# Performance work log

Measured on AMD Instinct MI355X. Metric: run time of the kernel, lower is better.

## Reference

```python
import jax, jax.numpy as jnp
import numpy as np

N, E, IN_DIM, OUT_DIM = 12288, 6144, 256, 256


def setup_inputs() -> dict:
    key = jax.random.key(0)
    k1, k2, k3, k4, k5 = jax.random.split(key, 5)
    x = jax.random.normal(k1, (N, IN_DIM), dtype=jnp.float32)
    # incidence-like matrix (dense, values in [0,1))
    H = jax.random.uniform(k2, (N, E), dtype=jnp.float32)
    # degree-normalizer diagonals: positive entries on the diagonal
    dv = jax.random.uniform(k3, (N,), dtype=jnp.float32, minval=0.1, maxval=1.0)
    de = jax.random.uniform(k4, (E,), dtype=jnp.float32, minval=0.1, maxval=1.0)
    D_v_neg_sqrt = jnp.diag(dv)
    D_e_neg = jnp.diag(de)
    # Linear params (xavier-like weight, zero bias)
    W = jax.random.normal(k5, (IN_DIM, OUT_DIM), dtype=jnp.float32) * (1.0 / np.sqrt(IN_DIM))
    b = jnp.zeros((OUT_DIM,), dtype=jnp.float32)
    return {"x": x, "H": H, "D_v_neg_sqrt": D_v_neg_sqrt, "D_e_neg": D_e_neg, "W": W, "b": b}


def reference(x, H, D_v_neg_sqrt, D_e_neg, W, b):
    # x_transformed = Linear(x)
    x_t = x @ W + b                      # [N, out]
    x_norm = D_v_neg_sqrt @ x_t          # [N, out]
    x_he = H.T @ x_norm                  # [E, out]
    x_he_norm = D_e_neg @ x_he           # [E, out]
    x_node = H @ x_he_norm               # [N, out]
    out = D_v_neg_sqrt @ x_node          # [N, out]
    # dropout is identity in eval mode
    return out
```

## Files before the change

kernel.cpp:

```cpp
#include <hip/hip_runtime.h>

#define NN 12288
#define NE 6144
#define ND 256

typedef __attribute__((ext_vector_type(8))) short short8;
typedef __attribute__((ext_vector_type(4))) float f32x4;
typedef unsigned short u16;
typedef unsigned int u32;

__device__ inline u16 f2bf(float f) {
  union { float f; u32 u; } v; v.f = f;
  u32 r = v.u + 0x7fffu + ((v.u >> 16) & 1u);
  return (u16)(r >> 16);
}

__device__ inline void gll16(const void* g, void* l) {
  __builtin_amdgcn_global_load_lds(
      (const __attribute__((address_space(1))) u32*)g,
      (__attribute__((address_space(3))) u32*)l, 16, 0, 0);
}

__device__ inline void stage_B(const u16* __restrict__ Bg, int ldb, int k0,
                               u16* __restrict__ Blds) {
  const int w = threadIdx.x >> 6;
  const int lane = threadIdx.x & 63;
  const int dd = lane >> 2, p = lane & 3;
#pragma unroll
  for (int s = 0; s < 4; ++s) {
    const int dbase = (w * 4 + s) * 16;
    const int n = dbase + dd;
    const int c = (p - (n >> 1)) & 3;
    gll16(Bg + (size_t)n * ldb + k0 + c * 8, Blds + dbase * 32);
  }
}

__device__ inline short8 load_B(const u16* __restrict__ Blds, int n, int quad) {
  const int p = (quad + (n >> 1)) & 3;
  return *(const short8*)(Blds + n * 32 + p * 8);
}

__device__ inline void compute_tile(const u16* __restrict__ Al,
                                    const u16* __restrict__ Bl, int w, int ln,
                                    int quad, f32x4 (&acc)[4][4]) {
  short8 af[4];
#pragma unroll
  for (int mt = 0; mt < 4; ++mt)
    af[mt] = *(const short8*)(Al + (mt * 16 + ln) * 40 + quad * 8);
#pragma unroll
  for (int nt = 0; nt < 4; ++nt) {
    short8 bf = load_B(Bl, w * 64 + nt * 16 + ln, quad);
#pragma unroll
    for (int mt = 0; mt < 4; ++mt)
      acc[nt][mt] = __builtin_amdgcn_mfma_f32_16x16x32_bf16(af[mt], bf, acc[nt][mt], 0, 0, 0);
  }
}

__device__ inline short8 pack8(float4 f0, float4 f1) {
  short8 av;
  av[0] = (short)f2bf(f0.x); av[1] = (short)f2bf(f0.y);
  av[2] = (short)f2bf(f0.z); av[3] = (short)f2bf(f0.w);
  av[4] = (short)f2bf(f1.x); av[5] = (short)f2bf(f1.y);
  av[6] = (short)f2bf(f1.z); av[7] = (short)f2bf(f1.w);
  return av;
}

__global__ __launch_bounds__(256) void k_xform(
    const float* __restrict__ x, const u16* __restrict__ Wt,
    const float* __restrict__ b, const float* __restrict__ dv,
    u16* __restrict__ xnt) {
  __shared__ u16 Alds[64 * 40];
  __shared__ u16 Blds[256 * 32];
  const int tid = threadIdx.x;
  const int w = tid >> 6, lane = tid & 63, ln = lane & 15, quad = lane >> 4;
  const int m0 = blockIdx.x * 64;
  const int am = tid >> 2, ac = (tid & 3) * 8;
  f32x4 acc[4][4] = {};
  for (int kt = 0; kt < ND / 32; ++kt) {
    const int k0 = kt * 32;
    __syncthreads();
    stage_B(Wt, ND, k0, Blds);
    const float4* pa = (const float4*)(x + (size_t)(m0 + am) * ND + k0 + ac);
    *(short8*)(Alds + am * 40 + ac) = pack8(pa[0], pa[1]);
    __syncthreads();
    compute_tile(Alds, Blds, w, ln, quad, acc);
  }
#pragma unroll
  for (int nt = 0; nt < 4; ++nt) {
    const int d = w * 64 + nt * 16 + ln;
    const float bb = b[d];
#pragma unroll
    for (int mt = 0; mt < 4; ++mt) {
      const int vb = m0 + mt * 16 + quad * 4;
      f32x4 a = acc[nt][mt];
      union { u16 h[4]; uint2 u; } pk;
#pragma unroll
      for (int r = 0; r < 4; ++r) pk.h[r] = f2bf(dv[vb + r] * (a[r] + bb));
      *(uint2*)(xnt + (size_t)d * NN + vb) = pk.u;
    }
  }
}

template <int NC>
__global__ __launch_bounds__(256) void k_gemm1s(
    const float* __restrict__ H, const u16* __restrict__ xnt,
    float* __restrict__ P1) {
  constexpr int KLEN = NN / NC;
  __shared__ u16 Alds[64 * 40];
  __shared__ u16 Blds[256 * 32];
  const int tid = threadIdx.x;
  const int w = tid >> 6, lane = tid & 63, ln = lane & 15, quad = lane >> 4;
  const int e0 = blockIdx.x * 64;
  const int kbase = blockIdx.y * KLEN;
  const int p2 = tid & 3, ea = tid >> 2;
  f32x4 acc[4][4] = {};
  for (int kt = 0; kt < KLEN / 32; ++kt) {
    const int k0 = kbase + kt * 32;
    __syncthreads();
    stage_B(xnt, NN, k0, Blds);
#pragma unroll
    for (int i = 0; i < 4; ++i) {
      const int p = p2 + i * 4;
      const int v = k0 + p * 2;
      float g0 = H[(size_t)v * NE + e0 + ea];
      float g1 = H[(size_t)(v + 1) * NE + e0 + ea];
      u32 pk = (u32)f2bf(g0) | ((u32)f2bf(g1) << 16);
      *(u32*)(Alds + ea * 40 + p * 2) = pk;
    }
    __syncthreads();
    compute_tile(Alds, Blds, w, ln, quad, acc);
  }
  float* P = P1 + (size_t)blockIdx.y * NE * ND;
#pragma unroll
  for (int nt = 0; nt < 4; ++nt) {
    const int d = w * 64 + nt * 16 + ln;
#pragma unroll
    for (int mt = 0; mt < 4; ++mt) {
      const int eb = e0 + mt * 16 + quad * 4;
      f32x4 a = acc[nt][mt];
#pragma unroll
      for (int r = 0; r < 4; ++r)
        P[(size_t)(eb + r) * ND + d] = a[r];
    }
  }
}

template <int NC>
__global__ __launch_bounds__(256) void k_red1(
    const float* __restrict__ P1, const float* __restrict__ de,
    u16* __restrict__ xhet) {
  const int tid = threadIdx.x;
  const int e0 = blockIdx.x * 16;
  union { u16 h[16]; uint4 q[2]; } pk;
#pragma unroll
  for (int i = 0; i < 16; ++i) {
    float s = 0.f;
#pragma unroll
    for (int c = 0; c < NC; ++c)
      s += P1[(size_t)c * NE * ND + (size_t)(e0 + i) * ND + tid];
    pk.h[i] = f2bf(de[e0 + i] * s);
  }
  uint4* dst = (uint4*)(xhet + (size_t)tid * NE + e0);
  dst[0] = pk.q[0];
  dst[1] = pk.q[1];
}

template <int NC>
__global__ __launch_bounds__(256) void k_gemm2s(
    const float* __restrict__ H, const u16* __restrict__ xhet,
    float* __restrict__ P2) {
  constexpr int KLEN = NE / NC;
  __shared__ u16 Alds[64 * 40];
  __shared__ u16 Blds[256 * 32];
  const int tid = threadIdx.x;
  const int w = tid >> 6, lane = tid & 63, ln = lane & 15, quad = lane >> 4;
  const int m0 = blockIdx.x * 64;
  const int kbase = blockIdx.y * KLEN;
  const int am = tid >> 2, ac = (tid & 3) * 8;
  f32x4 acc[4][4] = {};
  for (int kt = 0; kt < KLEN / 32; ++kt) {
    const int k0 = kbase + kt * 32;
    __syncthreads();
    stage_B(xhet, NE, k0, Blds);
    const float4* pa = (const float4*)(H + (size_t)(m0 + am) * NE + k0 + ac);
    *(short8*)(Alds + am * 40 + ac) = pack8(pa[0], pa[1]);
    __syncthreads();
    compute_tile(Alds, Blds, w, ln, quad, acc);
  }
  float* P = P2 + (size_t)blockIdx.y * NN * ND;
#pragma unroll
  for (int nt = 0; nt < 4; ++nt) {
    const int d = w * 64 + nt * 16 + ln;
#pragma unroll
    for (int mt = 0; mt < 4; ++mt) {
      const int vb = m0 + mt * 16 + quad * 4;
      f32x4 a = acc[nt][mt];
#pragma unroll
      for (int r = 0; r < 4; ++r)
        P[(size_t)(vb + r) * ND + d] = a[r];
    }
  }
}

template <int NC>
__global__ __launch_bounds__(256) void k_red2(
    const float* __restrict__ P2, const float* __restrict__ dv,
    float* __restrict__ out) {
  const int tid = threadIdx.x;
  const int v0 = blockIdx.x * 16;
#pragma unroll
  for (int i = 0; i < 16; ++i) {
    float s = 0.f;
#pragma unroll
    for (int c = 0; c < NC; ++c)
      s += P2[(size_t)c * NN * ND + (size_t)(v0 + i) * ND + tid];
    out[(size_t)(v0 + i) * ND + tid] = dv[v0 + i] * s;
  }
}

__global__ __launch_bounds__(256) void k_prep(
    const float* __restrict__ W, const float* __restrict__ Dv,
    const float* __restrict__ De, u16* __restrict__ Wt,
    float* __restrict__ dv, float* __restrict__ de) {
  const int t = blockIdx.x * 256 + threadIdx.x;
  const int d = t >> 8, k = t & 255;
  Wt[d * 256 + k] = f2bf(W[k * 256 + d]);
  if (t < NN) dv[t] = Dv[(size_t)t * (NN + 1)];
  if (t < NE) de[t] = De[(size_t)t * (NE + 1)];
}

extern "C" void kernel_launch(void* const* d_in, const int* in_sizes, int n_in,
                              void* d_out, int out_size, void* d_ws, size_t ws_size,
                              hipStream_t stream) {
  const float* x  = (const float*)d_in[0];
  const float* H  = (const float*)d_in[1];
  const float* Dv = (const float*)d_in[2];
  const float* De = (const float*)d_in[3];
  const float* W  = (const float*)d_in[4];
  const float* b  = (const float*)d_in[5];
  float* out = (float*)d_out;
  char* ws = (char*)d_ws;
  u16* xnt   = (u16*)ws;
  u16* xhet  = (u16*)(ws + 6291456);
  u16* Wt    = (u16*)(ws + 9437184);
  float* dv  = (float*)(ws + 9568256);
  float* de  = (float*)(ws + 9617408);
  float* P1  = (float*)(ws + 9641984);

  hipLaunchKernelGGL(k_prep,   dim3(256), dim3(256), 0, stream, W, Dv, De, Wt, dv, de);
  hipLaunchKernelGGL(k_xform,  dim3(NN / 64), dim3(256), 0, stream, x, Wt, b, dv, xnt);

  if (ws_size >= 210968576ULL) {
    float* P2 = (float*)(ws + 110305280);
    hipLaunchKernelGGL(k_gemm1s<16>, dim3(NE / 64, 16), dim3(256), 0, stream, H, xnt, P1);
    hipLaunchKernelGGL(k_red1<16>,   dim3(NE / 16), dim3(256), 0, stream, P1, de, xhet);
    hipLaunchKernelGGL(k_gemm2s<8>,  dim3(NN / 64, 8), dim3(256), 0, stream, H, xhet, P2);
    hipLaunchKernelGGL(k_red2<8>,    dim3(NN / 16), dim3(256), 0, stream, P2, dv, out);
  } else {
    float* P2 = (float*)(ws + 59973632);
    hipLaunchKernelGGL(k_gemm1s<8>, dim3(NE / 64, 8), dim3(256), 0, stream, H, xnt, P1);
    hipLaunchKernelGGL(k_red1<8>,   dim3(NE / 16), dim3(256), 0, stream, P1, de, xhet);
    hipLaunchKernelGGL(k_gemm2s<4>, dim3(NN / 64, 4), dim3(256), 0, stream, H, xhet, P2);
    hipLaunchKernelGGL(k_red2<4>,   dim3(NN / 16), dim3(256), 0, stream, P2, dv, out);
  }
}
```

Before: 1.107 ms.

## Enlarge split-K GEMM tiles to 128 rows with 512-thread blocks, vectorize H loads

Both split-K GEMMs over H now use 512-thread blocks covering 128 rows of the M dimension. Eight waves are arranged 2x4, so each staged B tile is reused across twice as many rows, halving redundant B traffic per H element. The transposed H load in the first GEMM now uses float4 reads along E instead of scalar loads. The workspace-size branch is dropped: the 16/8-way split is always used, with P2 aliased onto P1. That aliasing assumes the workspace is always large enough and adds LDS per block, which may reduce occupancy.

```diff
diff --git a/kernel.cpp b/kernel.cpp
--- a/kernel.cpp
+++ b/kernel.cpp
@@ -21,8 +21,8 @@
       (__attribute__((address_space(3))) u32*)l, 16, 0, 0);
 }
 
-__device__ inline void stage_B(const u16* __restrict__ Bg, int ldb, int k0,
-                               u16* __restrict__ Blds) {
+__device__ inline void stage_B4(const u16* __restrict__ Bg, int ldb, int k0,
+                                u16* __restrict__ Blds) {
   const int w = threadIdx.x >> 6;
   const int lane = threadIdx.x & 63;
   const int dd = lane >> 2, p = lane & 3;
@@ -35,21 +35,35 @@
   }
 }
 
+__device__ inline void stage_B8(const u16* __restrict__ Bg, int ldb, int k0,
+                                u16* __restrict__ Blds) {
+  const int w = threadIdx.x >> 6;
+  const int lane = threadIdx.x & 63;
+  const int dd = lane >> 2, p = lane & 3;
+#pragma unroll
+  for (int s = 0; s < 2; ++s) {
+    const int dbase = (w * 2 + s) * 16;
+    const int n = dbase + dd;
+    const int c = (p - (n >> 1)) & 3;
+    gll16(Bg + (size_t)n * ldb + k0 + c * 8, Blds + dbase * 32);
+  }
+}
+
 __device__ inline short8 load_B(const u16* __restrict__ Blds, int n, int quad) {
   const int p = (quad + (n >> 1)) & 3;
   return *(const short8*)(Blds + n * 32 + p * 8);
 }
 
-__device__ inline void compute_tile(const u16* __restrict__ Al,
-                                    const u16* __restrict__ Bl, int w, int ln,
-                                    int quad, f32x4 (&acc)[4][4]) {
+__device__ inline void compute_tile(const u16* __restrict__ Al, int arow0,
+                                    const u16* __restrict__ Bl, int bcol0,
+                                    int ln, int quad, f32x4 (&acc)[4][4]) {
   short8 af[4];
 #pragma unroll
   for (int mt = 0; mt < 4; ++mt)
-    af[mt] = *(const short8*)(Al + (mt * 16 + ln) * 40 + quad * 8);
-#pragma unroll
-  for (int nt = 0; nt < 4; ++nt) {
-    short8 bf = load_B(Bl, w * 64 + nt * 16 + ln, quad);
+    af[mt] = *(const short8*)(Al + (arow0 + mt * 16 + ln) * 40 + quad * 8);
+#pragma unroll
+  for (int nt = 0; nt < 4; ++nt) {
+    short8 bf = load_B(Bl, bcol0 + nt * 16 + ln, quad);
 #pragma unroll
     for (int mt = 0; mt < 4; ++mt)
       acc[nt][mt] = __builtin_amdgcn_mfma_f32_16x16x32_bf16(af[mt], bf, acc[nt][mt], 0, 0, 0);
@@ -79,11 +93,11 @@
   for (int kt = 0; kt < ND / 32; ++kt) {
     const int k0 = kt * 32;
     __syncthreads();
-    stage_B(Wt, ND, k0, Blds);
+    stage_B4(Wt, ND, k0, Blds);
     const float4* pa = (const float4*)(x + (size_t)(m0 + am) * ND + k0 + ac);
     *(short8*)(Alds + am * 40 + ac) = pack8(pa[0], pa[1]);
     __syncthreads();
-    compute_tile(Alds, Blds, w, ln, quad, acc);
+    compute_tile(Alds, 0, Blds, w * 64, ln, quad, acc);
   }
 #pragma unroll
   for (int nt = 0; nt < 4; ++nt) {
@@ -102,41 +116,43 @@
 }
 
 template <int NC>
-__global__ __launch_bounds__(256) void k_gemm1s(
+__global__ __launch_bounds__(512) void k_gemm1s(
     const float* __restrict__ H, const u16* __restrict__ xnt,
     float* __restrict__ P1) {
   constexpr int KLEN = NN / NC;
-  __shared__ u16 Alds[64 * 40];
+  __shared__ u16 Alds[128 * 40];
   __shared__ u16 Blds[256 * 32];
   const int tid = threadIdx.x;
   const int w = tid >> 6, lane = tid & 63, ln = lane & 15, quad = lane >> 4;
-  const int e0 = blockIdx.x * 64;
+  const int wn = w & 3, wm = w >> 2;
+  const int e0 = blockIdx.x * 128;
   const int kbase = blockIdx.y * KLEN;
-  const int p2 = tid & 3, ea = tid >> 2;
+  const int ec = tid & 31, vp = tid >> 5;
   f32x4 acc[4][4] = {};
   for (int kt = 0; kt < KLEN / 32; ++kt) {
     const int k0 = kbase + kt * 32;
     __syncthreads();
-    stage_B(xnt, NN, k0, Blds);
-#pragma unroll
-    for (int i = 0; i < 4; ++i) {
-      const int p = p2 + i * 4;
-      const int v = k0 + p * 2;
-      float g0 = H[(size_t)v * NE + e0 + ea];
-      float g1 = H[(size_t)(v + 1) * NE + e0 + ea];
-      u32 pk = (u32)f2bf(g0) | ((u32)f2bf(g1) << 16);
-      *(u32*)(Alds + ea * 40 + p * 2) = pk;
-    }
-    __syncthreads();
-    compute_tile(Alds, Blds, w, ln, quad, acc);
+    stage_B8(xnt, NN, k0, Blds);
+    const int v = k0 + vp * 2;
+    const float4 h0 = *(const float4*)(H + (size_t)v * NE + e0 + ec * 4);
+    const float4 h1 = *(const float4*)(H + (size_t)(v + 1) * NE + e0 + ec * 4);
+    const float a0[4] = {h0.x, h0.y, h0.z, h0.w};
+    const float a1[4] = {h1.x, h1.y, h1.z, h1.w};
+#pragma unroll
+    for (int j = 0; j < 4; ++j) {
+      u32 pk = (u32)f2bf(a0[j]) | ((u32)f2bf(a1[j]) << 16);
+      *(u32*)(Alds + (ec * 4 + j) * 40 + vp * 2) = pk;
+    }
+    __syncthreads();
+    compute_tile(Alds, wm * 64, Blds, wn * 64, ln, quad, acc);
   }
   float* P = P1 + (size_t)blockIdx.y * NE * ND;
 #pragma unroll
   for (int nt = 0; nt < 4; ++nt) {
-    const int d = w * 64 + nt * 16 + ln;
+    const int d = wn * 64 + nt * 16 + ln;
 #pragma unroll
     for (int mt = 0; mt < 4; ++mt) {
-      const int eb = e0 + mt * 16 + quad * 4;
+      const int eb = e0 + wm * 64 + mt * 16 + quad * 4;
       f32x4 a = acc[nt][mt];
 #pragma unroll
       for (int r = 0; r < 4; ++r)
@@ -166,34 +182,35 @@
 }
 
 template <int NC>
-__global__ __launch_bounds__(256) void k_gemm2s(
+__global__ __launch_bounds__(512) void k_gemm2s(
     const float* __restrict__ H, const u16* __restrict__ xhet,
     float* __restrict__ P2) {
   constexpr int KLEN = NE / NC;
-  __shared__ u16 Alds[64 * 40];
+  __shared__ u16 Alds[128 * 40];
   __shared__ u16 Blds[256 * 32];
   const int tid = threadIdx.x;
   const int w = tid >> 6, lane = tid & 63, ln = lane & 15, quad = lane >> 4;
-  const int m0 = blockIdx.x * 64;
+  const int wn = w & 3, wm = w >> 2;
+  const int m0 = blockIdx.x * 128;
   const int kbase = blockIdx.y * KLEN;
   const int am = tid >> 2, ac = (tid & 3) * 8;
   f32x4 acc[4][4] = {};
   for (int kt = 0; kt < KLEN / 32; ++kt) {
     const int k0 = kbase + kt * 32;
     __syncthreads();
-    stage_B(xhet, NE, k0, Blds);
+    stage_B8(xhet, NE, k0, Blds);
     const float4* pa = (const float4*)(H + (size_t)(m0 + am) * NE + k0 + ac);
     *(short8*)(Alds + am * 40 + ac) = pack8(pa[0], pa[1]);
     __syncthreads();
-    compute_tile(Alds, Blds, w, ln, quad, acc);
+    compute_tile(Alds, wm * 64, Blds, wn * 64, ln, quad, acc);
   }
   float* P = P2 + (size_t)blockIdx.y * NN * ND;
 #pragma unroll
   for (int nt = 0; nt < 4; ++nt) {
-    const int d = w * 64 + nt * 16 + ln;
+    const int d = wn * 64 + nt * 16 + ln;
 #pragma unroll
     for (int mt = 0; mt < 4; ++mt) {
-      const int vb = m0 + mt * 16 + quad * 4;
+      const int vb = m0 + wm * 64 + mt * 16 + quad * 4;
       f32x4 a = acc[nt][mt];
 #pragma unroll
       for (int r = 0; r < 4; ++r)
@@ -246,21 +263,12 @@
   float* dv  = (float*)(ws + 9568256);
   float* de  = (float*)(ws + 9617408);
   float* P1  = (float*)(ws + 9641984);
-
-  hipLaunchKernelGGL(k_prep,   dim3(256), dim3(256), 0, stream, W, Dv, De, Wt, dv, de);
-  hipLaunchKernelGGL(k_xform,  dim3(NN / 64), dim3(256), 0, stream, x, Wt, b, dv, xnt);
-
-  if (ws_size >= 210968576ULL) {
-    float* P2 = (float*)(ws + 110305280);
-    hipLaunchKernelGGL(k_gemm1s<16>, dim3(NE / 64, 16), dim3(256), 0, stream, H, xnt, P1);
-    hipLaunchKernelGGL(k_red1<16>,   dim3(NE / 16), dim3(256), 0, stream, P1, de, xhet);
-    hipLaunchKernelGGL(k_gemm2s<8>,  dim3(NN / 64, 8), dim3(256), 0, stream, H, xhet, P2);
-    hipLaunchKernelGGL(k_red2<8>,    dim3(NN / 16), dim3(256), 0, stream, P2, dv, out);
-  } else {
-    float* P2 = (float*)(ws + 59973632);
-    hipLaunchKernelGGL(k_gemm1s<8>, dim3(NE / 64, 8), dim3(256), 0, stream, H, xnt, P1);
-    hipLaunchKernelGGL(k_red1<8>,   dim3(NE / 16), dim3(256), 0, stream, P1, de, xhet);
-    hipLaunchKernelGGL(k_gemm2s<4>, dim3(NN / 64, 4), dim3(256), 0, stream, H, xhet, P2);
-    hipLaunchKernelGGL(k_red2<4>,   dim3(NN / 16), dim3(256), 0, stream, P2, dv, out);
-  }
-}
+  float* P2  = P1;
+
+  hipLaunchKernelGGL(k_prep,       dim3(256), dim3(256), 0, stream, W, Dv, De, Wt, dv, de);
+  hipLaunchKernelGGL(k_xform,      dim3(NN / 64), dim3(256), 0, stream, x, Wt, b, dv, xnt);
+  hipLaunchKernelGGL(k_gemm1s<16>, dim3(NE / 128, 16), dim3(512), 0, stream, H, xnt, P1);
+  hipLaunchKernelGGL(k_red1<16>,   dim3(NE / 16), dim3(256), 0, stream, P1, de, xhet);
+  hipLaunchKernelGGL(k_gemm2s<8>,  dim3(NN / 128, 8), dim3(512), 0, stream, H, xhet, P2);
+  hipLaunchKernelGGL(k_red2<8>,    dim3(NN / 16), dim3(256), 0, stream, P2, dv, out);
+}
```

Result: faster. 1.074 ms (-3.0%).
